# Kernel tuning notes

Hardware: AMD Instinct MI355X
Metric: run time of the kernel (lower is better)

## Reference

```python
import jax, jax.numpy as jnp
import numpy as np
import math

B, S, DIN, DOUT, H, L, R, E = 8, 512, 256, 256, 8, 4, 8, 65536
N = B * S  # graph nodes = all tokens
DEPTH = DOUT // H


def setup_inputs() -> dict:
    key = jax.random.key(0)
    ks = jax.random.split(key, 16)
    s_in = 1.0 / math.sqrt(DIN)
    s_out = 1.0 / math.sqrt(DOUT)
    return {
        "x": jax.random.normal(ks[0], (B, S, DIN), jnp.float32),
        # graph structure (constant ints)
        "edge_src": jax.random.randint(ks[1], (E,), 0, N),
        "edge_dst": jax.random.randint(ks[2], (E,), 0, N),
        "edge_type": jax.random.randint(ks[3], (E,), 0, R),
        # linear: input_size -> output_size
        "Wl": jax.random.normal(ks[4], (DOUT, DIN), jnp.float32) * s_in,
        "bl": jnp.zeros((DOUT,), jnp.float32),
        # relational GAT params per layer / relation
        "Wgat": jax.random.normal(ks[5], (L, R, DOUT, DOUT), jnp.float32) * s_out,
        "a_src": jax.random.normal(ks[6], (L, R, DOUT), jnp.float32) * s_out,
        "a_dst": jax.random.normal(ks[7], (L, R, DOUT), jnp.float32) * s_out,
        # linear1: output_size -> input_size
        "W1": jax.random.normal(ks[8], (DIN, DOUT), jnp.float32) * s_out,
        "b1": jnp.zeros((DIN,), jnp.float32),
        # Wq, Wk: input_size -> output_size
        "Wq": jax.random.normal(ks[9], (DOUT, DIN), jnp.float32) * s_in,
        "bq": jnp.zeros((DOUT,), jnp.float32),
        "Wk": jax.random.normal(ks[10], (DOUT, DIN), jnp.float32) * s_in,
        "bk": jnp.zeros((DOUT,), jnp.float32),
    }


def _segment_softmax(e, dst, n):
    m = jax.ops.segment_max(e, dst, num_segments=n)
    ex = jnp.exp(e - m[dst])
    denom = jax.ops.segment_sum(ex, dst, num_segments=n)
    return ex / (denom[dst] + 1e-16)


def _rgat(h, Wgat, a_src, a_dst, edge_src, edge_dst, edge_type):
    # h: [N, DOUT]
    for l in range(L):
        # per-relation transform of all nodes: [R, N, D]
        hr = jnp.einsum('nd,rde->rne', h, Wgat[l])
        msg = hr[edge_type, edge_src]  # [E, D] gather by (relation, src)
        logits = (jnp.sum(a_src[l][edge_type] * msg, axis=-1)
                  + jnp.sum(a_dst[l][edge_type] * h[edge_dst], axis=-1))
        alpha = _segment_softmax(jax.nn.leaky_relu(logits, 0.2), edge_dst, N)
        agg = jax.ops.segment_sum(alpha[:, None] * msg, edge_dst, num_segments=N)
        h = jax.nn.elu(agg)
    return h


def reference(x, edge_src, edge_dst, edge_type, Wl, bl, Wgat, a_src, a_dst,
              W1, b1, Wq, bq, Wk, bk):
    h = x @ Wl.T + bl                       # [B, S, DOUT]
    h = h.reshape(N, DOUT)
    h = _rgat(h, Wgat, a_src, a_dst, edge_src, edge_dst, edge_type)
    h = h.reshape(B, S, DOUT)
    h = h @ W1.T + b1                       # [B, S, DIN]
    q = (h @ Wq.T + bq).reshape(B, S, H, DEPTH).transpose(0, 2, 1, 3)
    k = (h @ Wk.T + bk).reshape(B, S, H, DEPTH).transpose(0, 2, 1, 3)
    attn = jnp.einsum('bhqd,bhkd->bhqk', q, k) / math.sqrt(DEPTH)
    return attn
```

## Files before the change

kernel.cpp:

```cpp
#include <hip/hip_runtime.h>
#include <math.h>

#define NN 4096
#define D 256
#define RR 8
#define LL 4
#define EE 65536
#define BB 8
#define SS 512
#define HH 8
#define RK 256
#define RN 2048

typedef short bf16x8 __attribute__((ext_vector_type(8)));
typedef float f32x4 __attribute__((ext_vector_type(4)));

__device__ __forceinline__ unsigned short f2bf(float f) {
  unsigned u = __float_as_uint(f);
  unsigned r = (u + 0x7fffu + ((u >> 16) & 1u)) >> 16;
  return (unsigned short)r;
}
__device__ __forceinline__ float bf2f(unsigned short s) {
  return __uint_as_float(((unsigned)s) << 16);
}

__device__ __forceinline__ void gload16(unsigned short* dst, const unsigned short* src) {
  __builtin_amdgcn_global_load_lds(
      (const __attribute__((address_space(1))) void*)src,
      (__attribute__((address_space(3))) void*)dst, 16, 0, 0);
}

template<int BM, int BN, bool F32OUT, bool SPLITOUT>
__global__ __launch_bounds__(256) void gemm_split(
    const unsigned short* __restrict__ Ah, const unsigned short* __restrict__ Al,
    const unsigned short* __restrict__ Bh, const unsigned short* __restrict__ Bl,
    const float* __restrict__ bias,
    float* __restrict__ C, unsigned short* __restrict__ Ch, unsigned short* __restrict__ Cl,
    int M, int N, int K)
{
  constexpr int MF = BM / 32;
  constexpr int NF = BN / 32;
  constexpr int ABUF = BM * 32;
  constexpr int BBUF = BN * 32;
  constexpr int BUFSZ = 2 * ABUF + 2 * BBUF;
  __shared__ unsigned short lds[2 * BUFSZ];

  const int t = threadIdx.x;
  const int lane = t & 63;
  const int w = t >> 6;
  const int wm = w >> 1, wn = w & 1;
  const int rb = blockIdx.y * BM;
  const int cb = blockIdx.x * BN;

  f32x4 acc[MF][NF];
#pragma unroll
  for (int m = 0; m < MF; ++m)
#pragma unroll
    for (int n = 0; n < NF; ++n)
      acc[m][n] = (f32x4){0.f, 0.f, 0.f, 0.f};

  const int srow = t >> 2;
  const int lslot = (t & 3) ^ ((srow >> 1) & 3);
  const unsigned short* gAh = Ah + (size_t)(rb + srow) * K + lslot * 8;
  const unsigned short* gAl = Al + (size_t)(rb + srow) * K + lslot * 8;
  const unsigned short* gBh = Bh + (size_t)(cb + srow) * K + lslot * 8;
  const unsigned short* gBl = Bl + (size_t)(cb + srow) * K + lslot * 8;

  auto stage = [&](int buf, int k0) {
    unsigned short* p = lds + buf * BUFSZ;
#pragma unroll
    for (int i = 0; i < BM / 64; ++i) {
      gload16(p + i * 2048 + t * 8,        gAh + (size_t)i * 64 * K + k0);
      gload16(p + ABUF + i * 2048 + t * 8, gAl + (size_t)i * 64 * K + k0);
    }
#pragma unroll
    for (int i = 0; i < BN / 64; ++i) {
      gload16(p + 2 * ABUF + i * 2048 + t * 8,        gBh + (size_t)i * 64 * K + k0);
      gload16(p + 2 * ABUF + BBUF + i * 2048 + t * 8, gBl + (size_t)i * 64 * K + k0);
    }
  };

  stage(0, 0);
  int cur = 0;
  for (int k0 = 0; k0 < K; k0 += 32) {
    __syncthreads();
    if (k0 + 32 < K) stage(cur ^ 1, k0 + 32);
    const unsigned short* p = lds + cur * BUFSZ;

    bf16x8 ah[MF], al[MF];
#pragma unroll
    for (int m = 0; m < MF; ++m) {
      int row = wm * (BM / 2) + m * 16 + (lane & 15);
      int off = row * 32 + (((lane >> 4) ^ ((row >> 1) & 3)) << 3);
      ah[m] = *(const bf16x8*)(p + off);
      al[m] = *(const bf16x8*)(p + ABUF + off);
    }
#pragma unroll
    for (int n = 0; n < NF; ++n) {
      int brow = wn * (BN / 2) + n * 16 + (lane & 15);
      int boff = brow * 32 + (((lane >> 4) ^ ((brow >> 1) & 3)) << 3);
      bf16x8 bh = *(const bf16x8*)(p + 2 * ABUF + boff);
      bf16x8 bl = *(const bf16x8*)(p + 2 * ABUF + BBUF + boff);
#pragma unroll
      for (int m = 0; m < MF; ++m) {
        acc[m][n] = __builtin_amdgcn_mfma_f32_16x16x32_bf16(ah[m], bh, acc[m][n], 0, 0, 0);
        acc[m][n] = __builtin_amdgcn_mfma_f32_16x16x32_bf16(al[m], bh, acc[m][n], 0, 0, 0);
        acc[m][n] = __builtin_amdgcn_mfma_f32_16x16x32_bf16(ah[m], bl, acc[m][n], 0, 0, 0);
      }
    }
    cur ^= 1;
  }

#pragma unroll
  for (int m = 0; m < MF; ++m) {
#pragma unroll
    for (int n = 0; n < NF; ++n) {
      int row0 = rb + wm * (BM / 2) + m * 16 + (lane >> 4) * 4;
      int col = cb + wn * (BN / 2) + n * 16 + (lane & 15);
      float bv = bias ? bias[col] : 0.f;
#pragma unroll
      for (int j = 0; j < 4; ++j) {
        float v = acc[m][n][j] + bv;
        size_t idx = (size_t)(row0 + j) * N + col;
        if (F32OUT) C[idx] = v;
        if (SPLITOUT) {
          unsigned short hb = f2bf(v);
          Ch[idx] = hb;
          Cl[idx] = f2bf(v - bf2f(hb));
        }
      }
    }
  }
}

__global__ __launch_bounds__(128, 1) void gemm_rgat(
    const unsigned short* __restrict__ Ah, const unsigned short* __restrict__ Al,
    const unsigned short* __restrict__ Bh, const unsigned short* __restrict__ Bl,
    float* __restrict__ C)
{
  constexpr int ABUF = 128 * 32;
  constexpr int BUFSZ = 4 * ABUF;
  __shared__ unsigned short lds[2 * BUFSZ];

  const int t = threadIdx.x;
  const int lane = t & 63;
  const int wm = t >> 6;
  const int rb = blockIdx.y * 128;
  const int cb = blockIdx.x * 128;

  f32x4 acc[4][8];
#pragma unroll
  for (int m = 0; m < 4; ++m)
#pragma unroll
    for (int n = 0; n < 8; ++n)
      acc[m][n] = (f32x4){0.f, 0.f, 0.f, 0.f};

  const int srow = t >> 2;
  const int lslot = (t & 3) ^ ((srow >> 1) & 3);
  const unsigned short* gAh = Ah + (size_t)(rb + srow) * RK + lslot * 8;
  const unsigned short* gAl = Al + (size_t)(rb + srow) * RK + lslot * 8;
  const unsigned short* gBh = Bh + (size_t)(cb + srow) * RK + lslot * 8;
  const unsigned short* gBl = Bl + (size_t)(cb + srow) * RK + lslot * 8;

  auto stage = [&](int buf, int k0) {
    unsigned short* p = lds + buf * BUFSZ;
#pragma unroll
    for (int i = 0; i < 4; ++i) {
      gload16(p + i * 1024 + t * 8,            gAh + (size_t)i * 32 * RK + k0);
      gload16(p + ABUF + i * 1024 + t * 8,     gAl + (size_t)i * 32 * RK + k0);
      gload16(p + 2 * ABUF + i * 1024 + t * 8, gBh + (size_t)i * 32 * RK + k0);
      gload16(p + 3 * ABUF + i * 1024 + t * 8, gBl + (size_t)i * 32 * RK + k0);
    }
  };

  stage(0, 0);
  int cur = 0;
  for (int k0 = 0; k0 < RK; k0 += 32) {
    __syncthreads();
    if (k0 + 32 < RK) stage(cur ^ 1, k0 + 32);
    const unsigned short* p = lds + cur * BUFSZ;

    bf16x8 ah[4], al[4];
#pragma unroll
    for (int m = 0; m < 4; ++m) {
      int row = wm * 64 + m * 16 + (lane & 15);
      int off = row * 32 + (((lane >> 4) ^ ((row >> 1) & 3)) << 3);
      ah[m] = *(const bf16x8*)(p + off);
      al[m] = *(const bf16x8*)(p + ABUF + off);
    }
#pragma unroll
    for (int n = 0; n < 8; ++n) {
      int brow = n * 16 + (lane & 15);
      int boff = brow * 32 + (((lane >> 4) ^ ((brow >> 1) & 3)) << 3);
      bf16x8 bh = *(const bf16x8*)(p + 2 * ABUF + boff);
      bf16x8 bl = *(const bf16x8*)(p + 3 * ABUF + boff);
#pragma unroll
      for (int m = 0; m < 4; ++m) {
        acc[m][n] = __builtin_amdgcn_mfma_f32_16x16x32_bf16(ah[m], bh, acc[m][n], 0, 0, 0);
        acc[m][n] = __builtin_amdgcn_mfma_f32_16x16x32_bf16(al[m], bh, acc[m][n], 0, 0, 0);
        acc[m][n] = __builtin_amdgcn_mfma_f32_16x16x32_bf16(ah[m], bl, acc[m][n], 0, 0, 0);
      }
    }
    cur ^= 1;
  }

#pragma unroll
  for (int m = 0; m < 4; ++m) {
#pragma unroll
    for (int n = 0; n < 8; ++n) {
      int row0 = rb + wm * 64 + m * 16 + (lane >> 4) * 4;
      int col = cb + n * 16 + (lane & 15);
#pragma unroll
      for (int j = 0; j < 4; ++j)
        C[(size_t)(row0 + j) * RN + col] = acc[m][n][j];
    }
  }
}

__global__ void count_k(const int* __restrict__ ed, int* __restrict__ cnt,
                        float* __restrict__ wa) {
  if (blockIdx.x < 32) wa[blockIdx.x * 256 + threadIdx.x] = 0.f;
  int e = blockIdx.x * 256 + threadIdx.x;
  if (e < EE) atomicAdd(&cnt[ed[e]], 1);
}

__global__ __launch_bounds__(1024) void scan_k(const int* __restrict__ cnt,
    int* __restrict__ off, int* __restrict__ cur) {
  __shared__ int part[1024];
  int t = threadIdx.x;
  int base = t * 4;
  int c0 = cnt[base], c1 = cnt[base+1], c2 = cnt[base+2], c3 = cnt[base+3];
  int s = c0 + c1 + c2 + c3;
  part[t] = s;
  __syncthreads();
  for (int o = 1; o < 1024; o <<= 1) {
    int v = 0;
    if (t >= o) v = part[t - o];
    __syncthreads();
    part[t] += v;
    __syncthreads();
  }
  int excl = part[t] - s;
  off[base] = excl; off[base+1] = excl + c0; off[base+2] = excl + c0 + c1;
  off[base+3] = excl + c0 + c1 + c2;
  cur[base] = excl; cur[base+1] = excl + c0; cur[base+2] = excl + c0 + c1;
  cur[base+3] = excl + c0 + c1 + c2;
  if (t == 1023) off[NN] = EE;
}

__global__ void fill_k(const int* __restrict__ ed, int* __restrict__ cur,
                       int* __restrict__ csr) {
  int e = blockIdx.x * 256 + threadIdx.x;
  if (e < EE) { int p = atomicAdd(&cur[ed[e]], 1); csr[p] = e; }
}

__global__ __launch_bounds__(256) void prep_k(
    const float* __restrict__ x, unsigned short* __restrict__ xh, unsigned short* __restrict__ xl,
    const float* __restrict__ Wl, unsigned short* __restrict__ wlh, unsigned short* __restrict__ wll,
    const float* __restrict__ Wq, const float* __restrict__ Wk, const float* __restrict__ W1,
    unsigned short* __restrict__ fqkh, unsigned short* __restrict__ fqkl,
    const float* __restrict__ b1, const float* __restrict__ bq, const float* __restrict__ bk,
    float* __restrict__ bqk,
    const float* __restrict__ Wgat, const float* __restrict__ asrc,
    unsigned short* __restrict__ th, unsigned short* __restrict__ tl,
    float* __restrict__ wa)
{
  __shared__ float s[32][33];
  int b = blockIdx.x, t = threadIdx.x;
  if (b < 1088) {
    const float* src; unsigned short* hi; unsigned short* lo; int i;
    if (b < 1024) { src = x;  hi = xh;  lo = xl;  i = b * 256 + t; }
    else          { src = Wl; hi = wlh; lo = wll; i = (b - 1024) * 256 + t; }
    float4 v = ((const float4*)src)[i];
    ushort4 h, l;
    h.x = f2bf(v.x); l.x = f2bf(v.x - bf2f(h.x));
    h.y = f2bf(v.y); l.y = f2bf(v.y - bf2f(h.y));
    h.z = f2bf(v.z); l.z = f2bf(v.z - bf2f(h.z));
    h.w = f2bf(v.w); l.w = f2bf(v.w - bf2f(h.w));
    ((ushort4*)hi)[i] = h;
    ((ushort4*)lo)[i] = l;
  } else if (b < 1600) {
    int b2 = b - 1088;
    int j = (b2 & 3) * 64 + (t & 63);
    int i = (b2 >> 2) * 4 + (t >> 6);
    const float* row = i < 256 ? Wq + (size_t)i * D : Wk + (size_t)(i - 256) * D;
    float sm = 0.f;
    for (int k = 0; k < D; ++k) sm += row[k] * W1[(size_t)k * D + j];
    size_t idx = (size_t)i * D + j;
    unsigned short hb = f2bf(sm);
    fqkh[idx] = hb;
    fqkl[idx] = f2bf(sm - bf2f(hb));
  } else if (b < 1728) {
    int b2 = b - 1600;
    int idx = b2 * 4 + (t >> 6);
    int lane = t & 63;
    const float* row = idx < 256 ? Wq + (size_t)idx * D : Wk + (size_t)(idx - 256) * D;
    float sm = 0.f;
    for (int i = lane; i < D; i += 64) sm += row[i] * b1[i];
#pragma unroll
    for (int o = 32; o; o >>= 1) sm += __shfl_down(sm, o);
    if (lane == 0) bqk[idx] = sm + (idx < 256 ? bq[idx] : bk[idx - 256]);
  } else {
    int b2 = b - 1728;
    int g = b2 >> 6, bi = (b2 >> 3) & 7, bj = b2 & 7;
    int r = t >> 3, c = (t & 7) * 4;
    float4 v = *(const float4*)(Wgat + ((size_t)g * D + bi * 32 + r) * D + bj * 32 + c);
    s[r][c + 0] = v.x; s[r][c + 1] = v.y; s[r][c + 2] = v.z; s[r][c + 3] = v.w;
    __syncthreads();
    size_t ob = ((size_t)g * D + bj * 32 + r) * D + bi * 32 + c;
    ushort4 h, l4;
    float o0 = s[c + 0][r], o1 = s[c + 1][r], o2 = s[c + 2][r], o3 = s[c + 3][r];
    h.x = f2bf(o0); l4.x = f2bf(o0 - bf2f(h.x));
    h.y = f2bf(o1); l4.y = f2bf(o1 - bf2f(h.y));
    h.z = f2bf(o2); l4.z = f2bf(o2 - bf2f(h.z));
    h.w = f2bf(o3); l4.w = f2bf(o3 - bf2f(h.w));
    *(ushort4*)(th + ob) = h;
    *(ushort4*)(tl + ob) = l4;
    if (t < 32) {
      const float* av = asrc + (size_t)g * D + bj * 32;
      float p2 = 0.f;
#pragma unroll
      for (int cc = 0; cc < 32; ++cc) p2 += s[t][cc] * av[cc];
      atomicAdd(&wa[(size_t)g * D + bi * 32 + t], p2);
    }
  }
}

__global__ __launch_bounds__(256) void scores_split_k(
    const unsigned short* __restrict__ hh, const unsigned short* __restrict__ hl,
    const float* __restrict__ wa_l, const float* __restrict__ adst_l,
    float* __restrict__ ssrc, float* __restrict__ sdst)
{
  __shared__ float sh[256];
  int n = blockIdx.x, tid = threadIdx.x;
  size_t idx = (size_t)n * D + tid;
  sh[tid] = bf2f(hh[idx]) + bf2f(hl[idx]);
  __syncthreads();
  int wv = tid >> 6, lane = tid & 63;
#pragma unroll
  for (int rr = 0; rr < 2; ++rr) {
    int r = wv * 2 + rr;
    const float* wr = wa_l + (size_t)r * D;
    const float* ar = adst_l + (size_t)r * D;
    float s1 = sh[lane] * wr[lane] + sh[lane+64] * wr[lane+64]
             + sh[lane+128] * wr[lane+128] + sh[lane+192] * wr[lane+192];
    float s2 = sh[lane] * ar[lane] + sh[lane+64] * ar[lane+64]
             + sh[lane+128] * ar[lane+128] + sh[lane+192] * ar[lane+192];
#pragma unroll
    for (int o = 32; o; o >>= 1) { s1 += __shfl_down(s1, o); s2 += __shfl_down(s2, o); }
    if (lane == 0) { ssrc[(size_t)r * NN + n] = s1; sdst[(size_t)r * NN + n] = s2; }
  }
}

__global__ __launch_bounds__(256) void agg_fused_k(
    const int* __restrict__ csr, const int* __restrict__ off,
    const int* __restrict__ et, const int* __restrict__ es,
    const float* __restrict__ ssrc, const float* __restrict__ sdst,
    const float* __restrict__ hr2,
    unsigned short* __restrict__ hh, unsigned short* __restrict__ hl,
    const float* __restrict__ wa_next, const float* __restrict__ adst_next,
    float* __restrict__ ssrc_o, float* __restrict__ sdst_o)
{
  __shared__ float slog[1024];
  __shared__ int soff[1024];
  __shared__ float sdn[RR];
  __shared__ float red[8];
  __shared__ float wred[4][256];
  int n = blockIdx.x, tid = threadIdx.x;
  int o0 = off[n];
  int deg = off[n + 1] - o0;
  if (deg > 1024) deg = 1024;
  if (tid < RR) sdn[tid] = sdst[(size_t)tid * NN + n];
  __syncthreads();
  for (int i = tid; i < deg; i += 256) {
    int e = csr[o0 + i];
    int t = et[e], s = es[e];
    float v = ssrc[(size_t)t * NN + s] + sdn[t];
    slog[i] = v > 0.f ? v : 0.2f * v;
    soff[i] = s * (RR * D) + t * D;
  }
  __syncthreads();
  int lane = tid & 63, wv = tid >> 6;
  float lm = -INFINITY;
  for (int i = tid; i < deg; i += 256) lm = fmaxf(lm, slog[i]);
#pragma unroll
  for (int o = 32; o; o >>= 1) lm = fmaxf(lm, __shfl_xor(lm, o));
  if (lane == 0) red[wv] = lm;
  __syncthreads();
  float m = fmaxf(fmaxf(red[0], red[1]), fmaxf(red[2], red[3]));
  float ls = 0.f;
  for (int i = tid; i < deg; i += 256) {
    float a = expf(slog[i] - m);
    slog[i] = a;
    ls += a;
  }
#pragma unroll
  for (int o = 32; o; o >>= 1) ls += __shfl_xor(ls, o);
  if (lane == 0) red[4 + wv] = ls;
  __syncthreads();
  float dinv = 1.f / (red[4] + red[5] + red[6] + red[7] + 1e-16f);
  float4 a4 = make_float4(0.f, 0.f, 0.f, 0.f);
  for (int i = wv; i < deg; i += 4) {
    float al = slog[i];
    float4 rv = ((const float4*)(hr2 + (size_t)soff[i]))[lane];
    a4.x += al * rv.x; a4.y += al * rv.y; a4.z += al * rv.z; a4.w += al * rv.w;
  }
  ((float4*)wred[wv])[lane] = a4;
  __syncthreads();
  float acc = (wred[0][tid] + wred[1][tid]) + (wred[2][tid] + wred[3][tid]);
  acc *= dinv;
  float v = acc > 0.f ? acc : expm1f(acc);
  size_t idx = (size_t)n * D + tid;
  unsigned short hb = f2bf(v);
  hh[idx] = hb;
  hl[idx] = f2bf(v - bf2f(hb));

  if (wa_next) {
    __syncthreads();
    slog[tid] = v;
    __syncthreads();
#pragma unroll
    for (int rr2 = 0; rr2 < 2; ++rr2) {
      int r = wv * 2 + rr2;
      const float* wr = wa_next + (size_t)r * D;
      const float* ar = adst_next + (size_t)r * D;
      float s1 = slog[lane] * wr[lane] + slog[lane+64] * wr[lane+64]
               + slog[lane+128] * wr[lane+128] + slog[lane+192] * wr[lane+192];
      float s2 = slog[lane] * ar[lane] + slog[lane+64] * ar[lane+64]
               + slog[lane+128] * ar[lane+128] + slog[lane+192] * ar[lane+192];
#pragma unroll
      for (int o = 32; o; o >>= 1) { s1 += __shfl_down(s1, o); s2 += __shfl_down(s2, o); }
      if (lane == 0) { ssrc_o[(size_t)r * NN + n] = s1; sdst_o[(size_t)r * NN + n] = s2; }
    }
  }
}

__global__ __launch_bounds__(256) void attn_mfma_k(
    const unsigned short* __restrict__ qkh, const unsigned short* __restrict__ qkl,
    float* __restrict__ out)
{
  int bh = blockIdx.y; int b = bh >> 3, hd = bh & 7;
  int rb = (blockIdx.x >> 3) * 64, cb = (blockIdx.x & 7) * 64;
  int t = threadIdx.x, lane = t & 63, w = t >> 6;
  int wm = w >> 1, wn = w & 1;
  int colq = hd * 32 + (lane >> 4) * 8;
  int colk = 256 + colq;
  int arow = b * SS + rb + wm * 32 + (lane & 15);
  int brow = b * SS + cb + wn * 32 + (lane & 15);

  bf16x8 aH[2], aL[2], bH[2], bL[2];
#pragma unroll
  for (int m = 0; m < 2; ++m) {
    size_t o1 = (size_t)(arow + m * 16) * 512 + colq;
    aH[m] = *(const bf16x8*)(qkh + o1);
    aL[m] = *(const bf16x8*)(qkl + o1);
    size_t o2 = (size_t)(brow + m * 16) * 512 + colk;
    bH[m] = *(const bf16x8*)(qkh + o2);
    bL[m] = *(const bf16x8*)(qkl + o2);
  }
  f32x4 acc[2][2];
#pragma unroll
  for (int m = 0; m < 2; ++m)
#pragma unroll
    for (int n = 0; n < 2; ++n) {
      acc[m][n] = (f32x4){0.f, 0.f, 0.f, 0.f};
      acc[m][n] = __builtin_amdgcn_mfma_f32_16x16x32_bf16(aH[m], bH[n], acc[m][n], 0, 0, 0);
      acc[m][n] = __builtin_amdgcn_mfma_f32_16x16x32_bf16(aL[m], bH[n], acc[m][n], 0, 0, 0);
      acc[m][n] = __builtin_amdgcn_mfma_f32_16x16x32_bf16(aH[m], bL[n], acc[m][n], 0, 0, 0);
    }
  const float scale = 0.17677669529663687f;
  size_t ob = (size_t)bh * SS * SS;
#pragma unroll
  for (int m = 0; m < 2; ++m)
#pragma unroll
    for (int n = 0; n < 2; ++n) {
      int row0 = rb + wm * 32 + m * 16 + (lane >> 4) * 4;
      int col = cb + wn * 32 + n * 16 + (lane & 15);
#pragma unroll
      for (int j = 0; j < 4; ++j)
        out[ob + (size_t)(row0 + j) * SS + col] = acc[m][n][j] * scale;
    }
}

extern "C" void kernel_launch(void* const* d_in, const int* in_sizes, int n_in,
                              void* d_out, int out_size, void* d_ws, size_t ws_size,
                              hipStream_t stream) {
  const float* x    = (const float*)d_in[0];
  const int*   es   = (const int*)d_in[1];
  const int*   ed   = (const int*)d_in[2];
  const int*   et   = (const int*)d_in[3];
  const float* Wl   = (const float*)d_in[4];
  const float* bl   = (const float*)d_in[5];
  const float* Wgat = (const float*)d_in[6];
  const float* asr  = (const float*)d_in[7];
  const float* adt  = (const float*)d_in[8];
  const float* W1   = (const float*)d_in[9];
  const float* b1   = (const float*)d_in[10];
  const float* Wq   = (const float*)d_in[11];
  const float* bq   = (const float*)d_in[12];
  const float* Wk   = (const float*)d_in[13];
  const float* bk   = (const float*)d_in[14];
  float* out = (float*)d_out;

  char* w = (char*)d_ws;
  size_t o = 0;
  auto alloc = [&](size_t bytes) { void* p = w + o; o += (bytes + 255) & ~(size_t)255; return p; };
  unsigned short* hh    = (unsigned short*)alloc((size_t)NN * D * 2);
  unsigned short* hl    = (unsigned short*)alloc((size_t)NN * D * 2);
  unsigned short* Wgt_h = (unsigned short*)alloc((size_t)LL * RR * D * D * 2);
  unsigned short* Wgt_l = (unsigned short*)alloc((size_t)LL * RR * D * D * 2);
  unsigned short* wlh   = (unsigned short*)alloc((size_t)D * D * 2);
  unsigned short* wll   = (unsigned short*)alloc((size_t)D * D * 2);
  unsigned short* fqkh  = (unsigned short*)alloc((size_t)2 * D * D * 2);
  unsigned short* fqkl  = (unsigned short*)alloc((size_t)2 * D * D * 2);
  float* bqk   = (float*)alloc((size_t)2 * D * 4);
  float* wa    = (float*)alloc((size_t)LL * RR * D * 4);
  float* ssrcA = (float*)alloc((size_t)RR * NN * 4);
  float* sdstA = (float*)alloc((size_t)RR * NN * 4);
  float* ssrcB = (float*)alloc((size_t)RR * NN * 4);
  float* sdstB = (float*)alloc((size_t)RR * NN * 4);
  int*   cnt   = (int*)alloc((size_t)NN * 4);
  int*   off   = (int*)alloc((size_t)(NN + 1) * 4);
  int*   cur   = (int*)alloc((size_t)NN * 4);
  int*   csr   = (int*)alloc((size_t)EE * 4);
  char* big = (char*)alloc((size_t)NN * RR * D * 4);
  float*          hr2 = (float*)big;
  unsigned short* xh  = (unsigned short*)big;
  unsigned short* xl  = (unsigned short*)(big + (size_t)NN * D * 2);
  unsigned short* qkh = (unsigned short*)big;
  unsigned short* qkl = (unsigned short*)(big + (size_t)NN * 512 * 2);

  hipMemsetAsync(cnt, 0, NN * sizeof(int), stream);
  count_k<<<EE / 256, 256, 0, stream>>>(ed, cnt, wa);
  scan_k<<<1, 1024, 0, stream>>>(cnt, off, cur);
  fill_k<<<EE / 256, 256, 0, stream>>>(ed, cur, csr);

  prep_k<<<3776, 256, 0, stream>>>(x, xh, xl, Wl, wlh, wll, Wq, Wk, W1,
                                   fqkh, fqkl, b1, bq, bk, bqk,
                                   Wgat, asr, Wgt_h, Wgt_l, wa);

  gemm_split<64, 64, false, true><<<dim3(4, 64), 256, 0, stream>>>(
      xh, xl, wlh, wll, bl, nullptr, hh, hl, NN, D, D);
  scores_split_k<<<NN, 256, 0, stream>>>(hh, hl, wa, adt, ssrcA, sdstA);

  for (int l = 0; l < LL; ++l) {
    gemm_rgat<<<dim3(RN / 128, NN / 128), 128, 0, stream>>>(
        hh, hl, Wgt_h + (size_t)l * RR * D * D, Wgt_l + (size_t)l * RR * D * D, hr2);
    const float* wan = (l < LL - 1) ? wa + (size_t)(l + 1) * RR * D : nullptr;
    const float* adn = (l < LL - 1) ? adt + (size_t)(l + 1) * RR * D : nullptr;
    const float* sin_ = (l & 1) ? ssrcB : ssrcA;
    const float* din_ = (l & 1) ? sdstB : sdstA;
    float* sou_ = (l & 1) ? ssrcA : ssrcB;
    float* dou_ = (l & 1) ? sdstA : sdstB;
    agg_fused_k<<<NN, 256, 0, stream>>>(csr, off, et, es, sin_, din_, hr2,
                                        hh, hl, wan, adn, sou_, dou_);
  }

  gemm_split<64, 64, false, true><<<dim3(8, 64), 256, 0, stream>>>(
      hh, hl, fqkh, fqkl, bqk, nullptr, qkh, qkl, NN, 512, D);

  attn_mfma_k<<<dim3(64, BB * HH), 256, 0, stream>>>(qkh, qkl, out);
}
```

Measured before the change: 226.3 us.

## Merge small setup kernels into combined launches to cut launch count

The edge-count pass is folded into prep_k as extra blocks, and one memset now clears both cnt and wa, which are made contiguous. The CSR fill is merged with the first linear GEMM into one launch, and the layer-0 score computation runs as extra blocks inside the first RGAT GEMM launch. This removes several kernel launches and lets independent work run alongside each other. In exchange, blocks of different work types share launch bounds and LDS, the score blocks now run with 128 threads instead of 256, and the merged kernels' register use follows the heavier branch.

```diff
diff --git a/kernel.cpp b/kernel.cpp
--- a/kernel.cpp
+++ b/kernel.cpp
@@ -31,7 +31,7 @@
 }
 
 template<int BM, int BN, bool F32OUT, bool SPLITOUT>
-__global__ __launch_bounds__(256) void gemm_split(
+__device__ __forceinline__ void gemm_body(unsigned short* lds, int bx, int by,
     const unsigned short* __restrict__ Ah, const unsigned short* __restrict__ Al,
     const unsigned short* __restrict__ Bh, const unsigned short* __restrict__ Bl,
     const float* __restrict__ bias,
@@ -43,14 +43,13 @@
   constexpr int ABUF = BM * 32;
   constexpr int BBUF = BN * 32;
   constexpr int BUFSZ = 2 * ABUF + 2 * BBUF;
-  __shared__ unsigned short lds[2 * BUFSZ];
 
   const int t = threadIdx.x;
   const int lane = t & 63;
   const int w = t >> 6;
   const int wm = w >> 1, wn = w & 1;
-  const int rb = blockIdx.y * BM;
-  const int cb = blockIdx.x * BN;
+  const int rb = by * BM;
+  const int cb = bx * BN;
 
   f32x4 acc[MF][NF];
 #pragma unroll
@@ -133,95 +132,148 @@
   }
 }
 
-__global__ __launch_bounds__(128, 1) void gemm_rgat(
+template<int BM, int BN, bool F32OUT, bool SPLITOUT>
+__global__ __launch_bounds__(256) void gemm_split(
     const unsigned short* __restrict__ Ah, const unsigned short* __restrict__ Al,
     const unsigned short* __restrict__ Bh, const unsigned short* __restrict__ Bl,
-    float* __restrict__ C)
+    const float* __restrict__ bias,
+    float* __restrict__ C, unsigned short* __restrict__ Ch, unsigned short* __restrict__ Cl,
+    int M, int N, int K)
+{
+  __shared__ unsigned short lds[2 * (2 * BM * 32 + 2 * BN * 32)];
+  gemm_body<BM, BN, F32OUT, SPLITOUT>(lds, blockIdx.x, blockIdx.y,
+      Ah, Al, Bh, Bl, bias, C, Ch, Cl, M, N, K);
+}
+
+__global__ __launch_bounds__(256) void fill_gemm1_k(
+    const int* __restrict__ ed, int* __restrict__ cur, int* __restrict__ csr,
+    const unsigned short* __restrict__ xh, const unsigned short* __restrict__ xl,
+    const unsigned short* __restrict__ wlh, const unsigned short* __restrict__ wll,
+    const float* __restrict__ bl,
+    unsigned short* __restrict__ hh, unsigned short* __restrict__ hl)
+{
+  __shared__ unsigned short lds[2 * (2 * 64 * 32 + 2 * 64 * 32)];
+  int b = blockIdx.x;
+  if (b < 256) {
+    int e = b * 256 + threadIdx.x;
+    int p = atomicAdd(&cur[ed[e]], 1);
+    csr[p] = e;
+  } else {
+    int b2 = b - 256;
+    gemm_body<64, 64, false, true>(lds, b2 & 3, b2 >> 2,
+        xh, xl, wlh, wll, bl, nullptr, hh, hl, NN, D, D);
+  }
+}
+
+__global__ __launch_bounds__(128, 1) void rgat_scores_k(
+    const unsigned short* __restrict__ Ah, const unsigned short* __restrict__ Al,
+    const unsigned short* __restrict__ Bh, const unsigned short* __restrict__ Bl,
+    float* __restrict__ C,
+    const float* __restrict__ wa_l, const float* __restrict__ adst_l,
+    float* __restrict__ ssrc, float* __restrict__ sdst)
 {
   constexpr int ABUF = 128 * 32;
   constexpr int BUFSZ = 4 * ABUF;
   __shared__ unsigned short lds[2 * BUFSZ];
 
+  const int b = blockIdx.x;
   const int t = threadIdx.x;
-  const int lane = t & 63;
-  const int wm = t >> 6;
-  const int rb = blockIdx.y * 128;
-  const int cb = blockIdx.x * 128;
-
-  f32x4 acc[4][8];
-#pragma unroll
-  for (int m = 0; m < 4; ++m)
-#pragma unroll
-    for (int n = 0; n < 8; ++n)
-      acc[m][n] = (f32x4){0.f, 0.f, 0.f, 0.f};
-
-  const int srow = t >> 2;
-  const int lslot = (t & 3) ^ ((srow >> 1) & 3);
-  const unsigned short* gAh = Ah + (size_t)(rb + srow) * RK + lslot * 8;
-  const unsigned short* gAl = Al + (size_t)(rb + srow) * RK + lslot * 8;
-  const unsigned short* gBh = Bh + (size_t)(cb + srow) * RK + lslot * 8;
-  const unsigned short* gBl = Bl + (size_t)(cb + srow) * RK + lslot * 8;
-
-  auto stage = [&](int buf, int k0) {
-    unsigned short* p = lds + buf * BUFSZ;
-#pragma unroll
-    for (int i = 0; i < 4; ++i) {
-      gload16(p + i * 1024 + t * 8,            gAh + (size_t)i * 32 * RK + k0);
-      gload16(p + ABUF + i * 1024 + t * 8,     gAl + (size_t)i * 32 * RK + k0);
-      gload16(p + 2 * ABUF + i * 1024 + t * 8, gBh + (size_t)i * 32 * RK + k0);
-      gload16(p + 3 * ABUF + i * 1024 + t * 8, gBl + (size_t)i * 32 * RK + k0);
-    }
-  };
-
-  stage(0, 0);
-  int cur = 0;
-  for (int k0 = 0; k0 < RK; k0 += 32) {
-    __syncthreads();
-    if (k0 + 32 < RK) stage(cur ^ 1, k0 + 32);
-    const unsigned short* p = lds + cur * BUFSZ;
-
-    bf16x8 ah[4], al[4];
+  if (b < 512) {
+    const int bx = b & 15, by = b >> 4;
+    const int lane = t & 63;
+    const int wm = t >> 6;
+    const int rb = by * 128;
+    const int cb = bx * 128;
+
+    f32x4 acc[4][8];
+#pragma unroll
+    for (int m = 0; m < 4; ++m)
+#pragma unroll
+      for (int n = 0; n < 8; ++n)
+        acc[m][n] = (f32x4){0.f, 0.f, 0.f, 0.f};
+
+    const int srow = t >> 2;
+    const int lslot = (t & 3) ^ ((srow >> 1) & 3);
+    const unsigned short* gAh = Ah + (size_t)(rb + srow) * RK + lslot * 8;
+    const unsigned short* gAl = Al + (size_t)(rb + srow) * RK + lslot * 8;
+    const unsigned short* gBh = Bh + (size_t)(cb + srow) * RK + lslot * 8;
+    const unsigned short* gBl = Bl + (size_t)(cb + srow) * RK + lslot * 8;
+
+    auto stage = [&](int buf, int k0) {
+      unsigned short* p = lds + buf * BUFSZ;
+#pragma unroll
+      for (int i = 0; i < 4; ++i) {
+        gload16(p + i * 1024 + t * 8,            gAh + (size_t)i * 32 * RK + k0);
+        gload16(p + ABUF + i * 1024 + t * 8,     gAl + (size_t)i * 32 * RK + k0);
+        gload16(p + 2 * ABUF + i * 1024 + t * 8, gBh + (size_t)i * 32 * RK + k0);
+        gload16(p + 3 * ABUF + i * 1024 + t * 8, gBl + (size_t)i * 32 * RK + k0);
+      }
+    };
+
+    stage(0, 0);
+    int cur = 0;
+    for (int k0 = 0; k0 < RK; k0 += 32) {
+      __syncthreads();
+      if (k0 + 32 < RK) stage(cur ^ 1, k0 + 32);
+      const unsigned short* p = lds + cur * BUFSZ;
+
+      bf16x8 ah[4], al[4];
+#pragma unroll
+      for (int m = 0; m < 4; ++m) {
+        int row = wm * 64 + m * 16 + (lane & 15);
+        int off = row * 32 + (((lane >> 4) ^ ((row >> 1) & 3)) << 3);
+        ah[m] = *(const bf16x8*)(p + off);
+        al[m] = *(const bf16x8*)(p + ABUF + off);
+      }
+#pragma unroll
+      for (int n = 0; n < 8; ++n) {
+        int brow = n * 16 + (lane & 15);
+        int boff = brow * 32 + (((lane >> 4) ^ ((brow >> 1) & 3)) << 3);
+        bf16x8 bh = *(const bf16x8*)(p + 2 * ABUF + boff);
+        bf16x8 bl = *(const bf16x8*)(p + 3 * ABUF + boff);
+#pragma unroll
+        for (int m = 0; m < 4; ++m) {
+          acc[m][n] = __builtin_amdgcn_mfma_f32_16x16x32_bf16(ah[m], bh, acc[m][n], 0, 0, 0);
+          acc[m][n] = __builtin_amdgcn_mfma_f32_16x16x32_bf16(al[m], bh, acc[m][n], 0, 0, 0);
+          acc[m][n] = __builtin_amdgcn_mfma_f32_16x16x32_bf16(ah[m], bl, acc[m][n], 0, 0, 0);
+        }
+      }
+      cur ^= 1;
+    }
+
 #pragma unroll
     for (int m = 0; m < 4; ++m) {
-      int row = wm * 64 + m * 16 + (lane & 15);
-      int off = row * 32 + (((lane >> 4) ^ ((row >> 1) & 3)) << 3);
-      ah[m] = *(const bf16x8*)(p + off);
-      al[m] = *(const bf16x8*)(p + ABUF + off);
-    }
-#pragma unroll
-    for (int n = 0; n < 8; ++n) {
-      int brow = n * 16 + (lane & 15);
-      int boff = brow * 32 + (((lane >> 4) ^ ((brow >> 1) & 3)) << 3);
-      bf16x8 bh = *(const bf16x8*)(p + 2 * ABUF + boff);
-      bf16x8 bl = *(const bf16x8*)(p + 3 * ABUF + boff);
-#pragma unroll
-      for (int m = 0; m < 4; ++m) {
-        acc[m][n] = __builtin_amdgcn_mfma_f32_16x16x32_bf16(ah[m], bh, acc[m][n], 0, 0, 0);
-        acc[m][n] = __builtin_amdgcn_mfma_f32_16x16x32_bf16(al[m], bh, acc[m][n], 0, 0, 0);
-        acc[m][n] = __builtin_amdgcn_mfma_f32_16x16x32_bf16(ah[m], bl, acc[m][n], 0, 0, 0);
+#pragma unroll
+      for (int n = 0; n < 8; ++n) {
+        int row0 = rb + wm * 64 + m * 16 + (lane >> 4) * 4;
+        int col = cb + n * 16 + (lane & 15);
+#pragma unroll
+        for (int j = 0; j < 4; ++j)
+          C[(size_t)(row0 + j) * RN + col] = acc[m][n][j];
       }
     }
-    cur ^= 1;
-  }
-
-#pragma unroll
-  for (int m = 0; m < 4; ++m) {
-#pragma unroll
-    for (int n = 0; n < 8; ++n) {
-      int row0 = rb + wm * 64 + m * 16 + (lane >> 4) * 4;
-      int col = cb + n * 16 + (lane & 15);
-#pragma unroll
-      for (int j = 0; j < 4; ++j)
-        C[(size_t)(row0 + j) * RN + col] = acc[m][n][j];
-    }
-  }
-}
-
-__global__ void count_k(const int* __restrict__ ed, int* __restrict__ cnt,
-                        float* __restrict__ wa) {
-  if (blockIdx.x < 32) wa[blockIdx.x * 256 + threadIdx.x] = 0.f;
-  int e = blockIdx.x * 256 + threadIdx.x;
-  if (e < EE) atomicAdd(&cnt[ed[e]], 1);
+  } else {
+    float* sh = (float*)lds;
+    int n = b - 512;
+    size_t idx = (size_t)n * D + t;
+    sh[t]       = bf2f(Ah[idx])       + bf2f(Al[idx]);
+    sh[t + 128] = bf2f(Ah[idx + 128]) + bf2f(Al[idx + 128]);
+    __syncthreads();
+    int lane = t & 63, wv = t >> 6;
+#pragma unroll
+    for (int rr = 0; rr < 4; ++rr) {
+      int r = wv * 4 + rr;
+      const float* wr = wa_l + (size_t)r * D;
+      const float* ar = adst_l + (size_t)r * D;
+      float s1 = sh[lane] * wr[lane] + sh[lane+64] * wr[lane+64]
+               + sh[lane+128] * wr[lane+128] + sh[lane+192] * wr[lane+192];
+      float s2 = sh[lane] * ar[lane] + sh[lane+64] * ar[lane+64]
+               + sh[lane+128] * ar[lane+128] + sh[lane+192] * ar[lane+192];
+#pragma unroll
+      for (int o = 32; o; o >>= 1) { s1 += __shfl_down(s1, o); s2 += __shfl_down(s2, o); }
+      if (lane == 0) { ssrc[(size_t)r * NN + n] = s1; sdst[(size_t)r * NN + n] = s2; }
+    }
+  }
 }
 
 __global__ __launch_bounds__(1024) void scan_k(const int* __restrict__ cnt,
@@ -248,12 +300,6 @@
   if (t == 1023) off[NN] = EE;
 }
 
-__global__ void fill_k(const int* __restrict__ ed, int* __restrict__ cur,
-                       int* __restrict__ csr) {
-  int e = blockIdx.x * 256 + threadIdx.x;
-  if (e < EE) { int p = atomicAdd(&cur[ed[e]], 1); csr[p] = e; }
-}
-
 __global__ __launch_bounds__(256) void prep_k(
     const float* __restrict__ x, unsigned short* __restrict__ xh, unsigned short* __restrict__ xl,
     const float* __restrict__ Wl, unsigned short* __restrict__ wlh, unsigned short* __restrict__ wll,
@@ -263,7 +309,8 @@
     float* __restrict__ bqk,
     const float* __restrict__ Wgat, const float* __restrict__ asrc,
     unsigned short* __restrict__ th, unsigned short* __restrict__ tl,
-    float* __restrict__ wa)
+    float* __restrict__ wa,
+    const int* __restrict__ ed, int* __restrict__ cnt)
 {
   __shared__ float s[32][33];
   int b = blockIdx.x, t = threadIdx.x;
@@ -300,7 +347,7 @@
 #pragma unroll
     for (int o = 32; o; o >>= 1) sm += __shfl_down(sm, o);
     if (lane == 0) bqk[idx] = sm + (idx < 256 ? bq[idx] : bk[idx - 256]);
-  } else {
+  } else if (b < 3776) {
     int b2 = b - 1728;
     int g = b2 >> 6, bi = (b2 >> 3) & 7, bj = b2 & 7;
     int r = t >> 3, c = (t & 7) * 4;
@@ -323,32 +370,9 @@
       for (int cc = 0; cc < 32; ++cc) p2 += s[t][cc] * av[cc];
       atomicAdd(&wa[(size_t)g * D + bi * 32 + t], p2);
     }
-  }
-}
-
-__global__ __launch_bounds__(256) void scores_split_k(
-    const unsigned short* __restrict__ hh, const unsigned short* __restrict__ hl,
-    const float* __restrict__ wa_l, const float* __restrict__ adst_l,
-    float* __restrict__ ssrc, float* __restrict__ sdst)
-{
-  __shared__ float sh[256];
-  int n = blockIdx.x, tid = threadIdx.x;
-  size_t idx = (size_t)n * D + tid;
-  sh[tid] = bf2f(hh[idx]) + bf2f(hl[idx]);
-  __syncthreads();
-  int wv = tid >> 6, lane = tid & 63;
-#pragma unroll
-  for (int rr = 0; rr < 2; ++rr) {
-    int r = wv * 2 + rr;
-    const float* wr = wa_l + (size_t)r * D;
-    const float* ar = adst_l + (size_t)r * D;
-    float s1 = sh[lane] * wr[lane] + sh[lane+64] * wr[lane+64]
-             + sh[lane+128] * wr[lane+128] + sh[lane+192] * wr[lane+192];
-    float s2 = sh[lane] * ar[lane] + sh[lane+64] * ar[lane+64]
-             + sh[lane+128] * ar[lane+128] + sh[lane+192] * ar[lane+192];
-#pragma unroll
-    for (int o = 32; o; o >>= 1) { s1 += __shfl_down(s1, o); s2 += __shfl_down(s2, o); }
-    if (lane == 0) { ssrc[(size_t)r * NN + n] = s1; sdst[(size_t)r * NN + n] = s2; }
+  } else {
+    int e = (b - 3776) * 256 + t;
+    atomicAdd(&cnt[ed[e]], 1);
   }
 }
 
@@ -514,12 +538,12 @@
   unsigned short* fqkh  = (unsigned short*)alloc((size_t)2 * D * D * 2);
   unsigned short* fqkl  = (unsigned short*)alloc((size_t)2 * D * D * 2);
   float* bqk   = (float*)alloc((size_t)2 * D * 4);
+  int*   cnt   = (int*)alloc((size_t)NN * 4);
   float* wa    = (float*)alloc((size_t)LL * RR * D * 4);
   float* ssrcA = (float*)alloc((size_t)RR * NN * 4);
   float* sdstA = (float*)alloc((size_t)RR * NN * 4);
   float* ssrcB = (float*)alloc((size_t)RR * NN * 4);
   float* sdstB = (float*)alloc((size_t)RR * NN * 4);
-  int*   cnt   = (int*)alloc((size_t)NN * 4);
   int*   off   = (int*)alloc((size_t)(NN + 1) * 4);
   int*   cur   = (int*)alloc((size_t)NN * 4);
   int*   csr   = (int*)alloc((size_t)EE * 4);
@@ -530,22 +554,19 @@
   unsigned short* qkh = (unsigned short*)big;
   unsigned short* qkl = (unsigned short*)(big + (size_t)NN * 512 * 2);
 
-  hipMemsetAsync(cnt, 0, NN * sizeof(int), stream);
-  count_k<<<EE / 256, 256, 0, stream>>>(ed, cnt, wa);
+  hipMemsetAsync(cnt, 0, (size_t)NN * 4 + (size_t)LL * RR * D * 4, stream);
+
+  prep_k<<<4032, 256, 0, stream>>>(x, xh, xl, Wl, wlh, wll, Wq, Wk, W1,
+                                   fqkh, fqkl, b1, bq, bk, bqk,
+                                   Wgat, asr, Wgt_h, Wgt_l, wa, ed, cnt);
   scan_k<<<1, 1024, 0, stream>>>(cnt, off, cur);
-  fill_k<<<EE / 256, 256, 0, stream>>>(ed, cur, csr);
-
-  prep_k<<<3776, 256, 0, stream>>>(x, xh, xl, Wl, wlh, wll, Wq, Wk, W1,
-                                   fqkh, fqkl, b1, bq, bk, bqk,
-                                   Wgat, asr, Wgt_h, Wgt_l, wa);
-
-  gemm_split<64, 64, false, true><<<dim3(4, 64), 256, 0, stream>>>(
-      xh, xl, wlh, wll, bl, nullptr, hh, hl, NN, D, D);
-  scores_split_k<<<NN, 256, 0, stream>>>(hh, hl, wa, adt, ssrcA, sdstA);
+  fill_gemm1_k<<<512, 256, 0, stream>>>(ed, cur, csr, xh, xl, wlh, wll, bl, hh, hl);
 
   for (int l = 0; l < LL; ++l) {
-    gemm_rgat<<<dim3(RN / 128, NN / 128), 128, 0, stream>>>(
-        hh, hl, Wgt_h + (size_t)l * RR * D * D, Wgt_l + (size_t)l * RR * D * D, hr2);
+    int grid = (l == 0) ? 512 + NN : 512;
+    rgat_scores_k<<<grid, 128, 0, stream>>>(
+        hh, hl, Wgt_h + (size_t)l * RR * D * D, Wgt_l + (size_t)l * RR * D * D,
+        hr2, wa, adt, ssrcA, sdstA);
     const float* wan = (l < LL - 1) ? wa + (size_t)(l + 1) * RR * D : nullptr;
     const float* adn = (l < LL - 1) ? adt + (size_t)(l + 1) * RR * D : nullptr;
     const float* sin_ = (l & 1) ? ssrcB : ssrcA;
```

Measured after the change: 229.3 us. No clear change (+1.3%).
